# Optimization experiments

Measured on AMD Instinct MI355X. Metric: run time of the kernel, lower is better.

Reference implementation:

```python
import jax, jax.numpy as jnp
import numpy as np

L, D, H, T, B = 4, 512, 8, 1024, 8
FF = 4 * D          # 2048
E = 2
EC = E * D          # 1024 conv channels
K = 31
W = 64              # attention window
DH = D // H
EPS = 1e-5


def _ln(x, g, b):
    m = jnp.mean(x, axis=-1, keepdims=True)
    v = jnp.mean((x - m) ** 2, axis=-1, keepdims=True)
    return (x - m) * jax.lax.rsqrt(v + EPS) * g + b


def setup_inputs() -> dict:
    key = jax.random.key(0)
    ks = iter(jax.random.split(key, 64))
    n = lambda shape, s=0.02: jax.random.normal(next(ks), shape, dtype=jnp.float32) * s
    inp = {
        'x': jax.random.normal(next(ks), (B, T, D), dtype=jnp.float32),
        # FFN1 (half residual)
        'ffn1_ln_g': jnp.ones((L, D)), 'ffn1_ln_b': jnp.zeros((L, D)),
        'ffn1_w1': n((L, D, FF)), 'ffn1_b1': jnp.zeros((L, FF)),
        'ffn1_w2': n((L, FF, D)), 'ffn1_b2': jnp.zeros((L, D)),
        # local MHSA
        'attn_ln_g': jnp.ones((L, D)), 'attn_ln_b': jnp.zeros((L, D)),
        'qkv_w': n((L, D, 3 * D)), 'qkv_b': jnp.zeros((L, 3 * D)),
        'outp_w': n((L, D, D)), 'outp_b': jnp.zeros((L, D)),
        # conv module
        'conv_ln_g': jnp.ones((L, D)), 'conv_ln_b': jnp.zeros((L, D)),
        'pw1_w': n((L, D, 2 * EC)), 'pw1_b': jnp.zeros((L, 2 * EC)),
        'dw_w': n((L, EC, 1, K), 0.1), 'dw_b': jnp.zeros((L, EC)),
        'gn_g': jnp.ones((L, EC)), 'gn_b': jnp.zeros((L, EC)),
        'pw2_w': n((L, EC, D)), 'pw2_b': jnp.zeros((L, D)),
        # FFN2 (half residual)
        'ffn2_ln_g': jnp.ones((L, D)), 'ffn2_ln_b': jnp.zeros((L, D)),
        'ffn2_w1': n((L, D, FF)), 'ffn2_b1': jnp.zeros((L, FF)),
        'ffn2_w2': n((L, FF, D)), 'ffn2_b2': jnp.zeros((L, D)),
        # per-block final LN and decoder final LN
        'blk_ln_g': jnp.ones((L, D)), 'blk_ln_b': jnp.zeros((L, D)),
        'final_ln_g': jnp.ones((D,)), 'final_ln_b': jnp.zeros((D,)),
    }
    return inp


def _forward(x, ffn1_ln_g, ffn1_ln_b, ffn1_w1, ffn1_b1, ffn1_w2, ffn1_b2,
             attn_ln_g, attn_ln_b, qkv_w, qkv_b, outp_w, outp_b,
             conv_ln_g, conv_ln_b, pw1_w, pw1_b, dw_w, dw_b, gn_g, gn_b, pw2_w, pw2_b,
             ffn2_ln_g, ffn2_ln_b, ffn2_w1, ffn2_b1, ffn2_w2, ffn2_b2,
             blk_ln_g, blk_ln_b, final_ln_g, final_ln_b):
    t = jnp.arange(T)
    local_ok = jnp.abs(t[:, None] - t[None, :]) <= (W // 2)   # [T,T] banded window mask
    scale = DH ** -0.5

    for l in range(L):
        # ---- FFN1 (half residual), SiLU ----
        h = _ln(x, ffn1_ln_g[l], ffn1_ln_b[l])
        h = jax.nn.silu(h @ ffn1_w1[l] + ffn1_b1[l]) @ ffn1_w2[l] + ffn1_b2[l]
        x = x + 0.5 * h

        # ---- local windowed MHSA ----
        a = _ln(x, attn_ln_g[l], attn_ln_b[l])
        qkv = (a @ qkv_w[l] + qkv_b[l]).reshape(B, T, 3, H, DH)
        q, k, v = (qkv[:, :, 0].transpose(0, 2, 1, 3),  # [B,H,T,DH]
                   qkv[:, :, 1].transpose(0, 2, 1, 3),
                   qkv[:, :, 2].transpose(0, 2, 1, 3))
        scores = jnp.einsum('bhqd,bhkd->bhqk', q, k) * scale
        scores = jnp.where(local_ok, scores, -jnp.inf)
        attn = jax.nn.softmax(scores, axis=-1)
        o = jnp.einsum('bhqk,bhkd->bhqd', attn, v)
        o = o.transpose(0, 2, 1, 3).reshape(B, T, D)
        x = x + (o @ outp_w[l] + outp_b[l])

        # ---- convolution module ----
        c = _ln(x, conv_ln_g[l], conv_ln_b[l])
        c = c @ pw1_w[l] + pw1_b[l]                 # [B,T,2EC]
        c = c[..., :EC] * jax.nn.sigmoid(c[..., EC:])  # GLU (channel halves)
        c = c.transpose(0, 2, 1)                    # [B,EC,T]
        c = jax.lax.conv_general_dilated(
            c, dw_w[l], window_strides=(1,), padding=[((K - 1) // 2, (K - 1) // 2)],
            dimension_numbers=('NCH', 'OIH', 'NCH'), feature_group_count=EC)
        c = c + dw_b[l][None, :, None]
        # GroupNorm(num_groups=1): normalize over (C,T) per sample
        m = jnp.mean(c, axis=(1, 2), keepdims=True)
        vv = jnp.mean((c - m) ** 2, axis=(1, 2), keepdims=True)
        c = (c - m) * jax.lax.rsqrt(vv + EPS) * gn_g[l][None, :, None] + gn_b[l][None, :, None]
        c = jax.nn.silu(c)
        c = c.transpose(0, 2, 1) @ pw2_w[l] + pw2_b[l]  # [B,T,D]
        x = x + c

        # ---- FFN2 (half residual) ----
        h = _ln(x, ffn2_ln_g[l], ffn2_ln_b[l])
        h = jax.nn.silu(h @ ffn2_w1[l] + ffn2_b1[l]) @ ffn2_w2[l] + ffn2_b2[l]
        x = x + 0.5 * h

        # ---- per-block final LayerNorm ----
        x = _ln(x, blk_ln_g[l], blk_ln_b[l])

    return _ln(x, final_ln_g, final_ln_b)


def reference(x, ffn1_ln_g, ffn1_ln_b, ffn1_w1, ffn1_b1, ffn1_w2, ffn1_b2,
              attn_ln_g, attn_ln_b, qkv_w, qkv_b, outp_w, outp_b,
              conv_ln_g, conv_ln_b, pw1_w, pw1_b, dw_w, dw_b, gn_g, gn_b, pw2_w, pw2_b,
              ffn2_ln_g, ffn2_ln_b, ffn2_w1, ffn2_b1, ffn2_w2, ffn2_b2,
              blk_ln_g, blk_ln_b, final_ln_g, final_ln_b):
    return _forward(x, ffn1_ln_g, ffn1_ln_b, ffn1_w1, ffn1_b1, ffn1_w2, ffn1_b2,
                    attn_ln_g, attn_ln_b, qkv_w, qkv_b, outp_w, outp_b,
                    conv_ln_g, conv_ln_b, pw1_w, pw1_b, dw_w, dw_b, gn_g, gn_b, pw2_w, pw2_b,
                    ffn2_ln_g, ffn2_ln_b, ffn2_w1, ffn2_b1, ffn2_w2, ffn2_b2,
                    blk_ln_g, blk_ln_b, final_ln_g, final_ln_b)
```

## Files before the change

kernel.cpp:

```cpp
#include <hip/hip_runtime.h>
#include <hip/hip_bf16.h>
#include <math.h>

#define L_ 4
#define D_ 512
#define H_ 8
#define T_ 1024
#define B_ 8
#define FF_ 2048
#define EC_ 1024
#define KW_ 31
#define DH_ 64
#define ROWS (B_*T_)

typedef __attribute__((ext_vector_type(8))) short short8;
typedef __attribute__((ext_vector_type(4))) float f32x4;
typedef __attribute__((ext_vector_type(4))) unsigned short ushort4v;

static __device__ __forceinline__ unsigned short f2bf(float f) {
  __hip_bfloat16 h = __float2bfloat16(f);
  unsigned short u;
  __builtin_memcpy(&u, &h, 2);
  return u;
}
static __device__ __forceinline__ float bf2f(unsigned short h) {
  union { unsigned u; float f; } v; v.u = ((unsigned)h) << 16;
  return v.f;
}
static __device__ __forceinline__ float sigm(float x) {
  return __builtin_amdgcn_rcpf(1.0f + __expf(-x));
}

#define GLDS(gp, lp) __builtin_amdgcn_global_load_lds( \
    (const __attribute__((address_space(1))) unsigned int*)(const void*)(gp), \
    (__attribute__((address_space(3))) unsigned int*)(void*)(lp), 16, 0, 0)

#define SW8(row, slot) ((slot) ^ (((row) ^ ((row) >> 3)) & 7))

__global__ __launch_bounds__(256) void ln_bf16_kernel(const float* __restrict__ x,
    const float* __restrict__ g, const float* __restrict__ b, unsigned short* __restrict__ y)
{
  int row = blockIdx.x * 4 + (threadIdx.x >> 6);
  int l = threadIdx.x & 63;
  const float* xr = x + (size_t)row * D_ + l * 8;
  float4 v0 = *(const float4*)xr;
  float4 v1 = *(const float4*)(xr + 4);
  float vv[8] = {v0.x, v0.y, v0.z, v0.w, v1.x, v1.y, v1.z, v1.w};
  float s = 0.f, s2 = 0.f;
#pragma unroll
  for (int j = 0; j < 8; ++j) { s += vv[j]; s2 += vv[j] * vv[j]; }
#pragma unroll
  for (int off = 32; off; off >>= 1) {
    s  += __shfl_xor(s,  off, 64);
    s2 += __shfl_xor(s2, off, 64);
  }
  float mean = s * (1.0f / D_);
  float var  = s2 * (1.0f / D_) - mean * mean;
  float r = __builtin_amdgcn_rsqf(var + 1e-5f);
  float4 g0 = *(const float4*)(g + l * 8);
  float4 g1 = *(const float4*)(g + l * 8 + 4);
  float4 b0 = *(const float4*)(b + l * 8);
  float4 b1 = *(const float4*)(b + l * 8 + 4);
  float gg[8] = {g0.x, g0.y, g0.z, g0.w, g1.x, g1.y, g1.z, g1.w};
  float bb[8] = {b0.x, b0.y, b0.z, b0.w, b1.x, b1.y, b1.z, b1.w};
  short8 o;
#pragma unroll
  for (int j = 0; j < 8; ++j) o[j] = (short)f2bf((vv[j] - mean) * r * gg[j] + bb[j]);
  *(short8*)(y + (size_t)row * D_ + l * 8) = o;
}

template<bool BF2>
__global__ __launch_bounds__(256) void ln_dual_kernel(const float* __restrict__ x,
    const float* __restrict__ g1, const float* __restrict__ b1,
    const float* __restrict__ g2, const float* __restrict__ b2,
    float* __restrict__ y1, void* __restrict__ y2)
{
  int row = blockIdx.x * 4 + (threadIdx.x >> 6);
  int l = threadIdx.x & 63;
  const float* xr = x + (size_t)row * D_ + l * 8;
  float4 v0 = *(const float4*)xr;
  float4 v1 = *(const float4*)(xr + 4);
  float vv[8] = {v0.x, v0.y, v0.z, v0.w, v1.x, v1.y, v1.z, v1.w};
  float s = 0.f, s2 = 0.f;
#pragma unroll
  for (int j = 0; j < 8; ++j) { s += vv[j]; s2 += vv[j] * vv[j]; }
#pragma unroll
  for (int off = 32; off; off >>= 1) {
    s  += __shfl_xor(s,  off, 64);
    s2 += __shfl_xor(s2, off, 64);
  }
  float mean = s * (1.0f / D_);
  float var  = s2 * (1.0f / D_) - mean * mean;
  float r = __builtin_amdgcn_rsqf(var + 1e-5f);
  float4 g0 = *(const float4*)(g1 + l * 8);
  float4 g1v = *(const float4*)(g1 + l * 8 + 4);
  float4 b0 = *(const float4*)(b1 + l * 8);
  float4 b1v = *(const float4*)(b1 + l * 8 + 4);
  float ga[8] = {g0.x, g0.y, g0.z, g0.w, g1v.x, g1v.y, g1v.z, g1v.w};
  float ba[8] = {b0.x, b0.y, b0.z, b0.w, b1v.x, b1v.y, b1v.z, b1v.w};
  float yv[8];
  float u = 0.f, u2 = 0.f;
#pragma unroll
  for (int j = 0; j < 8; ++j) {
    yv[j] = (vv[j] - mean) * r * ga[j] + ba[j];
    u += yv[j]; u2 += yv[j] * yv[j];
  }
  {
    float4 o0 = {yv[0], yv[1], yv[2], yv[3]};
    float4 o1 = {yv[4], yv[5], yv[6], yv[7]};
    float* yp = y1 + (size_t)row * D_ + l * 8;
    *(float4*)yp = o0; *(float4*)(yp + 4) = o1;
  }
#pragma unroll
  for (int off = 32; off; off >>= 1) {
    u  += __shfl_xor(u,  off, 64);
    u2 += __shfl_xor(u2, off, 64);
  }
  float mean2 = u * (1.0f / D_);
  float var2  = u2 * (1.0f / D_) - mean2 * mean2;
  float r2 = __builtin_amdgcn_rsqf(var2 + 1e-5f);
  float4 c0 = *(const float4*)(g2 + l * 8);
  float4 c1 = *(const float4*)(g2 + l * 8 + 4);
  float4 d0 = *(const float4*)(b2 + l * 8);
  float4 d1 = *(const float4*)(b2 + l * 8 + 4);
  float gc[8] = {c0.x, c0.y, c0.z, c0.w, c1.x, c1.y, c1.z, c1.w};
  float bc[8] = {d0.x, d0.y, d0.z, d0.w, d1.x, d1.y, d1.z, d1.w};
  if constexpr (BF2) {
    short8 o;
#pragma unroll
    for (int j = 0; j < 8; ++j) o[j] = (short)f2bf((yv[j] - mean2) * r2 * gc[j] + bc[j]);
    *(short8*)((unsigned short*)y2 + (size_t)row * D_ + l * 8) = o;
  } else {
    float z[8];
#pragma unroll
    for (int j = 0; j < 8; ++j) z[j] = (yv[j] - mean2) * r2 * gc[j] + bc[j];
    float4 o0 = {z[0], z[1], z[2], z[3]};
    float4 o1 = {z[4], z[5], z[6], z[7]};
    float* yp = (float*)y2 + (size_t)row * D_ + l * 8;
    *(float4*)yp = o0; *(float4*)(yp + 4) = o1;
  }
}

__global__ __launch_bounds__(256) void wtr_kernel(const float* __restrict__ W,
    unsigned short* __restrict__ Wt, int K, int N)
{
  __shared__ float tile[32][33];
  const float* Wl = W + (size_t)blockIdx.z * K * N;
  unsigned short* Wtl = Wt + (size_t)blockIdx.z * K * N;
  int n0 = blockIdx.x * 32, k0 = blockIdx.y * 32;
  int c = threadIdx.x & 31, r = threadIdx.x >> 5;
#pragma unroll
  for (int it = 0; it < 4; ++it) {
    int kk = r + it * 8;
    tile[kk][c] = Wl[(size_t)(k0 + kk) * N + n0 + c];
  }
  __syncthreads();
#pragma unroll
  for (int it = 0; it < 4; ++it) {
    int nn = r + it * 8;
    Wtl[(size_t)(n0 + nn) * K + k0 + c] = f2bf(tile[c][nn]);
  }
}

template<int EPI>
__global__ __launch_bounds__(256) void gemm_mfma(
    const unsigned short* __restrict__ A, const unsigned short* __restrict__ Wt,
    const float* __restrict__ bias, void* __restrict__ Cv,
    int N, int K)
{
  constexpr int TM = 128;
  constexpr int AI = TM / 32;
  __shared__ __align__(16) unsigned short As[3][TM * 32];
  __shared__ __align__(16) unsigned short Bs[3][128 * 32];
  int t = threadIdx.x;
  int gx = gridDim.x;
  int nwg = gx * gridDim.y;
  int orig = blockIdx.y * gx + blockIdx.x;
  int lg = (orig & 7) * (nwg >> 3) + (orig >> 3);
  int row0 = (lg / gx) * TM;
  int col0 = (lg % gx) * (EPI == 3 ? 64 : 128);
  int l = t & 63, w = t >> 6, wm = w >> 1, wn = w & 1;

  int ar0 = t >> 2;
  int sa0 = (t & 3) ^ ((ar0 >> 1) & 3);
  int ar1 = (t + 256) >> 2;
  int sa1 = (t & 3) ^ ((ar1 >> 1) & 3);
  const unsigned short* agp0 = A + (size_t)(row0 + ar0) * K + sa0 * 8;
  const unsigned short* agp1 = A + (size_t)(row0 + ar1) * K + sa1 * 8;
  const unsigned short* bgp0 = Wt + (size_t)(col0 + ar0) * K + sa0 * 8;
  const unsigned short* bgp1 =
      (EPI == 3) ? Wt + (size_t)(EC_ + col0 + (ar1 - 64)) * K + sa1 * 8
                 : Wt + (size_t)(col0 + ar1) * K + sa1 * 8;

  int lrow = (l >> 4) * 4, lcol = l & 15, kq = l >> 4;
  int aoff[AI], boff[4];
#pragma unroll
  for (int i = 0; i < AI; ++i) {
    int row = wm * (TM / 2) + i * 16 + lcol;
    aoff[i] = (row * 4 + (kq ^ ((row >> 1) & 3))) * 8;
  }
#pragma unroll
  for (int j = 0; j < 4; ++j) {
    int row;
    if constexpr (EPI == 3)
      row = (j < 2 ? wn * 32 + j * 16 : 64 + wn * 32 + (j - 2) * 16) + lcol;
    else
      row = wn * 64 + j * 16 + lcol;
    boff[j] = (row * 4 + (kq ^ ((row >> 1) & 3))) * 8;
  }

  f32x4 acc[AI][4] = {};
  int nt = K >> 5;

  auto stage = [&](int buf) {
    GLDS(agp0, As[buf] + t * 8);
    GLDS(agp1, As[buf] + (t + 256) * 8);
    GLDS(bgp0, Bs[buf] + t * 8);
    GLDS(bgp1, Bs[buf] + (t + 256) * 8);
    agp0 += 32; agp1 += 32; bgp0 += 32; bgp1 += 32;
  };
  stage(0); stage(1);
  int cur = 0, nxt = 2;

  for (int kt = 0; kt < nt; ++kt) {
    if (kt < nt - 1) asm volatile("s_waitcnt vmcnt(4)" ::: "memory");
    else             asm volatile("s_waitcnt vmcnt(0)" ::: "memory");
    __builtin_amdgcn_s_barrier();
    __builtin_amdgcn_sched_barrier(0);
    if (kt + 2 < nt) { stage(nxt); nxt = (nxt == 2) ? 0 : nxt + 1; }
    const unsigned short* Ab = As[cur];
    const unsigned short* Bb = Bs[cur];
    cur = (cur == 2) ? 0 : cur + 1;
    short8 af[AI], bfr[4];
#pragma unroll
    for (int i = 0; i < AI; ++i) af[i]  = *(const short8*)(Ab + aoff[i]);
#pragma unroll
    for (int j = 0; j < 4; ++j) bfr[j] = *(const short8*)(Bb + boff[j]);
    __builtin_amdgcn_s_setprio(1);
#pragma unroll
    for (int i = 0; i < AI; ++i)
#pragma unroll
      for (int j = 0; j < 4; ++j)
        acc[i][j] = __builtin_amdgcn_mfma_f32_16x16x32_bf16(af[i], bfr[j], acc[i][j], 0, 0, 0);
    __builtin_amdgcn_s_setprio(0);
  }

  if constexpr (EPI == 3) {
    float bja[2], bjg[2];
#pragma unroll
    for (int j = 0; j < 2; ++j) {
      int c = col0 + wn * 32 + j * 16 + lcol;
      bja[j] = bias[c];
      bjg[j] = bias[EC_ + c];
    }
#pragma unroll
    for (int i = 0; i < AI; ++i) {
      int gr0 = row0 + wm * (TM / 2) + i * 16 + lrow;
#pragma unroll
      for (int j = 0; j < 2; ++j) {
        int gc = col0 + wn * 32 + j * 16 + lcol;
#pragma unroll
        for (int q = 0; q < 4; ++q) {
          float a = acc[i][j][q] + bja[j];
          float g = acc[i][j + 2][q] + bjg[j];
          ((unsigned short*)Cv)[(size_t)(gr0 + q) * N + gc] = f2bf(a * sigm(g));
        }
      }
    }
  } else {
    float bj[4];
#pragma unroll
    for (int j = 0; j < 4; ++j) bj[j] = bias[col0 + wn * 64 + j * 16 + lcol];
#pragma unroll
    for (int i = 0; i < AI; ++i) {
      int gr0 = row0 + wm * (TM / 2) + i * 16 + lrow;
#pragma unroll
      for (int j = 0; j < 4; ++j) {
        int gc = col0 + wn * 64 + j * 16 + lcol;
#pragma unroll
        for (int q = 0; q < 4; ++q) {
          float v = acc[i][j][q] + bj[j];
          size_t off = (size_t)(gr0 + q) * N + gc;
          if constexpr (EPI == 0) {
            ((unsigned short*)Cv)[off] = f2bf(v);
          } else {
            ((unsigned short*)Cv)[off] = f2bf(v * sigm(v));
          }
        }
      }
    }
  }
}

__global__ __launch_bounds__(256) void gemm_res64(
    const unsigned short* __restrict__ A, const unsigned short* __restrict__ Wt,
    const float* __restrict__ bias, const float* __restrict__ R, float* __restrict__ C,
    int N, int K, float alpha)
{
  __shared__ __align__(16) unsigned short As[3][64 * 64];
  __shared__ __align__(16) unsigned short Bs[3][128 * 64];
  int t = threadIdx.x;
  int gx = gridDim.x;
  int nwg = gx * gridDim.y;
  int orig = blockIdx.y * gx + blockIdx.x;
  int lg = (orig & 7) * (nwg >> 3) + (orig >> 3);
  int row0 = (lg / gx) * 64;
  int col0 = (lg % gx) * 128;
  int l = t & 63, w = t >> 6, wm = w >> 1, wn = w & 1;

  int arA0 = t >> 3;
  int sA0  = (t & 7) ^ (arA0 & 7);
  int cA1  = t + 256;
  int arA1 = cA1 >> 3;
  int sA1  = (cA1 & 7) ^ (arA1 & 7);
  const unsigned short* agp0 = A + (size_t)(row0 + arA0) * K + sA0 * 8;
  const unsigned short* agp1 = A + (size_t)(row0 + arA1) * K + sA1 * 8;
  const unsigned short* bgp[4];
#pragma unroll
  for (int q = 0; q < 4; ++q) {
    int c = t + q * 256;
    int r = c >> 3, s = (c & 7) ^ (r & 7);
    bgp[q] = Wt + (size_t)(col0 + r) * K + s * 8;
  }

  int lcol = l & 15, kq = l >> 4, lrow = kq * 4;
  int aoff[2][2], boff[4][2];
#pragma unroll
  for (int i = 0; i < 2; ++i) {
    int row = wm * 32 + i * 16 + lcol;
#pragma unroll
    for (int kk = 0; kk < 2; ++kk)
      aoff[i][kk] = row * 64 + (((kk * 4 + kq) ^ (row & 7)) * 8);
  }
#pragma unroll
  for (int j = 0; j < 4; ++j) {
    int row = wn * 64 + j * 16 + lcol;
#pragma unroll
    for (int kk = 0; kk < 2; ++kk)
      boff[j][kk] = row * 64 + (((kk * 4 + kq) ^ (row & 7)) * 8);
  }

  f32x4 acc[2][4] = {};
  int nt = K >> 6;

  auto stage = [&](int buf) {
    GLDS(agp0, As[buf] + t * 8);
    GLDS(agp1, As[buf] + (t + 256) * 8);
#pragma unroll
    for (int q = 0; q < 4; ++q) GLDS(bgp[q], Bs[buf] + (t + q * 256) * 8);
    agp0 += 64; agp1 += 64;
#pragma unroll
    for (int q = 0; q < 4; ++q) bgp[q] += 64;
  };
  stage(0); stage(1);
  int cur = 0, nxt = 2;

  for (int kt = 0; kt < nt; ++kt) {
    if (kt < nt - 1) asm volatile("s_waitcnt vmcnt(6)" ::: "memory");
    else             asm volatile("s_waitcnt vmcnt(0)" ::: "memory");
    __builtin_amdgcn_s_barrier();
    __builtin_amdgcn_sched_barrier(0);
    if (kt + 2 < nt) { stage(nxt); nxt = (nxt == 2) ? 0 : nxt + 1; }
    const unsigned short* Ab = As[cur];
    const unsigned short* Bb = Bs[cur];
    cur = (cur == 2) ? 0 : cur + 1;
    short8 af[2][2], bfr[4][2];
#pragma unroll
    for (int i = 0; i < 2; ++i)
#pragma unroll
      for (int kk = 0; kk < 2; ++kk) af[i][kk] = *(const short8*)(Ab + aoff[i][kk]);
#pragma unroll
    for (int j = 0; j < 4; ++j)
#pragma unroll
      for (int kk = 0; kk < 2; ++kk) bfr[j][kk] = *(const short8*)(Bb + boff[j][kk]);
    __builtin_amdgcn_s_setprio(1);
#pragma unroll
    for (int kk = 0; kk < 2; ++kk)
#pragma unroll
      for (int i = 0; i < 2; ++i)
#pragma unroll
        for (int j = 0; j < 4; ++j)
          acc[i][j] = __builtin_amdgcn_mfma_f32_16x16x32_bf16(af[i][kk], bfr[j][kk],
                                                              acc[i][j], 0, 0, 0);
    __builtin_amdgcn_s_setprio(0);
  }

  float bj[4];
#pragma unroll
  for (int j = 0; j < 4; ++j) bj[j] = bias[col0 + wn * 64 + j * 16 + lcol];
#pragma unroll
  for (int i = 0; i < 2; ++i) {
    int gr0 = row0 + wm * 32 + i * 16 + lrow;
#pragma unroll
    for (int j = 0; j < 4; ++j) {
      int gc = col0 + wn * 64 + j * 16 + lcol;
#pragma unroll
      for (int q = 0; q < 4; ++q) {
        size_t off = (size_t)(gr0 + q) * N + gc;
        C[off] = R[off] + alpha * (acc[i][j][q] + bj[j]);
      }
    }
  }
}

__global__ __launch_bounds__(256) void attn_kernel(const unsigned short* __restrict__ QKV,
                                                   unsigned short* __restrict__ O)
{
  __shared__ __align__(16) unsigned short Ks[128 * 64];
  __shared__ __align__(16) unsigned short Vt[64 * 128];
  __shared__ __align__(16) unsigned short Ps[64 * 128];
  int qt = blockIdx.x, h = blockIdx.y, b = blockIdx.z;
  int t = threadIdx.x;
  int l = t & 63, w = t >> 6;
  int q0 = qt * 64;
  int jbase = q0 - 32;

#pragma unroll
  for (int i = 0; i < 4; ++i) {
    int c = t + i * 256;
    int row = c >> 3, sl = c & 7;
    int jg = jbase + row;
    short8 kv = {};
    if ((unsigned)jg < (unsigned)T_)
      kv = *(const short8*)(QKV + ((size_t)(b * T_ + jg)) * 1536 + 512 + h * DH_ + sl * 8);
    *(short8*)(Ks + row * 64 + SW8(row, sl) * 8) = kv;
  }
#pragma unroll
  for (int i = 0; i < 4; ++i) {
    int c = t + i * 256;
    int row = c >> 3, d0 = (c & 7) * 8;
    int jg = jbase + row;
    short8 vv = {};
    if ((unsigned)jg < (unsigned)T_)
      vv = *(const short8*)(QKV + ((size_t)(b * T_ + jg)) * 1536 + 1024 + h * DH_ + d0);
#pragma unroll
    for (int q = 0; q < 8; ++q) {
      int d = d0 + q;
      Vt[d * 128 + SW8(d, row >> 3) * 8 + (row & 7)] = (unsigned short)vv[q];
    }
  }
  short8 qf[2];
#pragma unroll
  for (int ks = 0; ks < 2; ++ks)
    qf[ks] = *(const short8*)(QKV + ((size_t)(b * T_ + q0 + w * 16 + (l & 15))) * 1536
                              + h * DH_ + ks * 32 + (l >> 4) * 8);
  __syncthreads();

  f32x4 sacc[8] = {};
#pragma unroll
  for (int jt = 0; jt < 8; ++jt) {
#pragma unroll
    for (int ks = 0; ks < 2; ++ks) {
      int row = jt * 16 + (l & 15);
      int sl = ks * 4 + (l >> 4);
      short8 kf = *(const short8*)(Ks + row * 64 + SW8(row, sl) * 8);
      sacc[jt] = __builtin_amdgcn_mfma_f32_16x16x32_bf16(qf[ks], kf, sacc[jt], 0, 0, 0);
    }
  }

  const float scale = 0.125f;
  int qgl0 = q0 + w * 16 + ((l >> 4) << 2);
  int jl = jbase + (l & 15);
  float m4[4] = {-3.0e38f, -3.0e38f, -3.0e38f, -3.0e38f};
#pragma unroll
  for (int jt = 0; jt < 8; ++jt) {
#pragma unroll
    for (int r = 0; r < 4; ++r) {
      float s = sacc[jt][r] * scale;
      int jg = jl + jt * 16;
      int dd = jg - (qgl0 + r);
      bool ok = ((unsigned)jg < (unsigned)T_) && (dd <= 32) && (dd >= -32);
      s = ok ? s : -3.0e38f;
      sacc[jt][r] = s;
      m4[r] = fmaxf(m4[r], s);
    }
  }
#pragma unroll
  for (int r = 0; r < 4; ++r) {
    m4[r] = fmaxf(m4[r], __shfl_xor(m4[r], 1, 64));
    m4[r] = fmaxf(m4[r], __shfl_xor(m4[r], 2, 64));
    m4[r] = fmaxf(m4[r], __shfl_xor(m4[r], 4, 64));
    m4[r] = fmaxf(m4[r], __shfl_xor(m4[r], 8, 64));
  }
  float sum4[4] = {0.f, 0.f, 0.f, 0.f};
#pragma unroll
  for (int jt = 0; jt < 8; ++jt) {
#pragma unroll
    for (int r = 0; r < 4; ++r) {
      float e = __expf(sacc[jt][r] - m4[r]);
      sum4[r] += e;
      int qrow = w * 16 + ((l >> 4) << 2) + r;
      int j = jt * 16 + (l & 15);
      Ps[qrow * 128 + SW8(qrow, j >> 3) * 8 + (j & 7)] = f2bf(e);
    }
  }
#pragma unroll
  for (int r = 0; r < 4; ++r) {
    sum4[r] += __shfl_xor(sum4[r], 1, 64);
    sum4[r] += __shfl_xor(sum4[r], 2, 64);
    sum4[r] += __shfl_xor(sum4[r], 4, 64);
    sum4[r] += __shfl_xor(sum4[r], 8, 64);
    sum4[r] = __builtin_amdgcn_rcpf(sum4[r]);
  }

  f32x4 oacc[4] = {};
#pragma unroll
  for (int ks = 0; ks < 4; ++ks) {
    int prow = w * 16 + (l & 15);
    int sl = ks * 4 + (l >> 4);
    short8 pf = *(const short8*)(Ps + prow * 128 + SW8(prow, sl) * 8);
#pragma unroll
    for (int dt = 0; dt < 4; ++dt) {
      int vrow = dt * 16 + (l & 15);
      short8 vf = *(const short8*)(Vt + vrow * 128 + SW8(vrow, sl) * 8);
      oacc[dt] = __builtin_amdgcn_mfma_f32_16x16x32_bf16(pf, vf, oacc[dt], 0, 0, 0);
    }
  }
#pragma unroll
  for (int dt = 0; dt < 4; ++dt) {
#pragma unroll
    for (int r = 0; r < 4; ++r) {
      int qg = q0 + w * 16 + ((l >> 4) << 2) + r;
      int d = dt * 16 + (l & 15);
      O[((size_t)(b * T_ + qg)) * D_ + h * DH_ + d] = f2bf(oacc[dt][r] * sum4[r]);
    }
  }
}

#define TT_ 16
__global__ __launch_bounds__(256) void dwconv_kernel(const unsigned short* __restrict__ X,
    const float* __restrict__ w, const float* __restrict__ bias, float* __restrict__ Y,
    float* __restrict__ red)
{
  int t = threadIdx.x;
  int gid = blockIdx.x;
  int ecb = gid & 3;
  int tt  = (gid >> 2) & 63;
  int b   = gid >> 8;
  int e  = ecb * 256 + t;
  int t0 = tt * TT_;
  const unsigned short* xp = X + (size_t)b * T_ * EC_ + e;

  float wr[KW_];
#pragma unroll
  for (int k = 0; k < KW_; ++k) wr[k] = w[e * KW_ + k];
  float out[TT_];
  float bv = bias[e];
#pragma unroll
  for (int i = 0; i < TT_; ++i) out[i] = bv;

#pragma unroll
  for (int j = 0; j < TT_ + KW_ - 1; ++j) {
    int tj = t0 - 15 + j;
    float xv = ((unsigned)tj < (unsigned)T_) ? bf2f(xp[(size_t)tj * EC_]) : 0.f;
#pragma unroll
    for (int i = 0; i < TT_; ++i) {
      int k = j - i;
      if (k >= 0 && k < KW_) out[i] = fmaf(xv, wr[k], out[i]);
    }
  }
  float* yp = Y + ((size_t)b * T_ + t0) * EC_ + e;
  float s = 0.f, s2 = 0.f;
#pragma unroll
  for (int i = 0; i < TT_; ++i) {
    yp[(size_t)i * EC_] = out[i];
    s += out[i]; s2 += out[i] * out[i];
  }
#pragma unroll
  for (int off = 32; off; off >>= 1) {
    s  += __shfl_down(s,  off, 64);
    s2 += __shfl_down(s2, off, 64);
  }
  __shared__ float rs[4], rq[4];
  if ((t & 63) == 0) { rs[t >> 6] = s; rq[t >> 6] = s2; }
  __syncthreads();
  if (t == 0) {
    int loc = gid & 255;
    red[(b * 256 + loc) * 2]     = rs[0] + rs[1] + rs[2] + rs[3];
    red[(b * 256 + loc) * 2 + 1] = rq[0] + rq[1] + rq[2] + rq[3];
  }
}

__global__ __launch_bounds__(256) void gn_stats_kernel(const float* __restrict__ partial,
                                                       float* __restrict__ stats)
{
  int b = blockIdx.x, t = threadIdx.x;
  float s  = partial[b * 512 + t * 2];
  float s2 = partial[b * 512 + t * 2 + 1];
#pragma unroll
  for (int off = 32; off; off >>= 1) {
    s  += __shfl_down(s,  off, 64);
    s2 += __shfl_down(s2, off, 64);
  }
  __shared__ float rs[4], rq[4];
  if ((t & 63) == 0) { rs[t >> 6] = s; rq[t >> 6] = s2; }
  __syncthreads();
  if (t == 0) {
    float S = rs[0] + rs[1] + rs[2] + rs[3];
    float S2 = rq[0] + rq[1] + rq[2] + rq[3];
    const float n = (float)(T_ * EC_);
    float mean = S / n;
    float var  = S2 / n - mean * mean;
    stats[b * 2]     = mean;
    stats[b * 2 + 1] = __builtin_amdgcn_rsqf(var + 1e-5f);
  }
}

__global__ __launch_bounds__(256) void gn_apply_kernel(const float* __restrict__ X,
    const float* __restrict__ stats, const float* __restrict__ g, const float* __restrict__ bb,
    unsigned short* __restrict__ out)
{
  int idx = blockIdx.x * 256 + threadIdx.x;
  int e4 = (idx & 255) << 2;
  int bt = idx >> 8;
  int b  = bt >> 10;
  float mean = stats[b * 2], rstd = stats[b * 2 + 1];
  float4 v  = *(const float4*)(X + (size_t)idx * 4);
  float4 gv = *(const float4*)(g + e4);
  float4 bv = *(const float4*)(bb + e4);
  float vv[4] = {v.x, v.y, v.z, v.w};
  float gg[4] = {gv.x, gv.y, gv.z, gv.w};
  float bbv[4] = {bv.x, bv.y, bv.z, bv.w};
  ushort4v o;
#pragma unroll
  for (int j = 0; j < 4; ++j) {
    float u = (vv[j] - mean) * rstd * gg[j] + bbv[j];
    o[j] = f2bf(u * sigm(u));
  }
  *(ushort4v*)(out + (size_t)idx * 4) = o;
}

extern "C" void kernel_launch(void* const* d_in, const int* in_sizes, int n_in,
                              void* d_out, int out_size, void* d_ws, size_t ws_size,
                              hipStream_t stream)
{
  const float* in_x      = (const float*)d_in[0];
  const float* ffn1_ln_g = (const float*)d_in[1];
  const float* ffn1_ln_b = (const float*)d_in[2];
  const float* ffn1_w1   = (const float*)d_in[3];
  const float* ffn1_b1   = (const float*)d_in[4];
  const float* ffn1_w2   = (const float*)d_in[5];
  const float* ffn1_b2   = (const float*)d_in[6];
  const float* attn_ln_g = (const float*)d_in[7];
  const float* attn_ln_b = (const float*)d_in[8];
  const float* qkv_w     = (const float*)d_in[9];
  const float* qkv_b     = (const float*)d_in[10];
  const float* outp_w    = (const float*)d_in[11];
  const float* outp_b    = (const float*)d_in[12];
  const float* conv_ln_g = (const float*)d_in[13];
  const float* conv_ln_b = (const float*)d_in[14];
  const float* pw1_w     = (const float*)d_in[15];
  const float* pw1_b     = (const float*)d_in[16];
  const float* dw_w      = (const float*)d_in[17];
  const float* dw_b      = (const float*)d_in[18];
  const float* gn_g      = (const float*)d_in[19];
  const float* gn_b      = (const float*)d_in[20];
  const float* pw2_w     = (const float*)d_in[21];
  const float* pw2_b     = (const float*)d_in[22];
  const float* ffn2_ln_g = (const float*)d_in[23];
  const float* ffn2_ln_b = (const float*)d_in[24];
  const float* ffn2_w1   = (const float*)d_in[25];
  const float* ffn2_b1   = (const float*)d_in[26];
  const float* ffn2_w2   = (const float*)d_in[27];
  const float* ffn2_b2   = (const float*)d_in[28];
  const float* blk_ln_g  = (const float*)d_in[29];
  const float* blk_ln_b  = (const float*)d_in[30];
  const float* fin_ln_g  = (const float*)d_in[31];
  const float* fin_ln_b  = (const float*)d_in[32];

  char* p = (char*)d_ws;
  float* x    = (float*)p;          p += (size_t)ROWS * D_ * 4;
  float* big3 = (float*)p;          p += (size_t)ROWS * EC_ * 4;
  float* red  = (float*)p;          p += 8192 * 4;
  unsigned short* abuf  = (unsigned short*)p; p += (size_t)ROWS * D_ * 2;
  unsigned short* inner = (unsigned short*)p; p += (size_t)ROWS * FF_ * 2;
  unsigned short* big2  = (unsigned short*)p; p += (size_t)ROWS * EC_ * 2;
  unsigned short* wt_w1a = (unsigned short*)p; p += (size_t)L_ * D_ * FF_ * 2;
  unsigned short* wt_w1b = (unsigned short*)p; p += (size_t)L_ * FF_ * D_ * 2;
  unsigned short* wt_qkv = (unsigned short*)p; p += (size_t)L_ * D_ * 1536 * 2;
  unsigned short* wt_out = (unsigned short*)p; p += (size_t)L_ * D_ * D_ * 2;
  unsigned short* wt_pw1 = (unsigned short*)p; p += (size_t)L_ * D_ * 2048 * 2;
  unsigned short* wt_pw2 = (unsigned short*)p; p += (size_t)L_ * EC_ * D_ * 2;
  unsigned short* wt_w2a = (unsigned short*)p; p += (size_t)L_ * D_ * FF_ * 2;
  unsigned short* wt_w2b = (unsigned short*)p; p += (size_t)L_ * FF_ * D_ * 2;
  float* stats = red + 4096;

  hipMemcpyAsync(x, in_x, sizeof(float) * (size_t)ROWS * D_,
                 hipMemcpyDeviceToDevice, stream);

  dim3 blk256(256);
  wtr_kernel<<<dim3(FF_/32,  D_/32,  L_), blk256, 0, stream>>>(ffn1_w1, wt_w1a, D_, FF_);
  wtr_kernel<<<dim3(D_/32,   FF_/32, L_), blk256, 0, stream>>>(ffn1_w2, wt_w1b, FF_, D_);
  wtr_kernel<<<dim3(1536/32, D_/32,  L_), blk256, 0, stream>>>(qkv_w,   wt_qkv, D_, 1536);
  wtr_kernel<<<dim3(D_/32,   D_/32,  L_), blk256, 0, stream>>>(outp_w,  wt_out, D_, D_);
  wtr_kernel<<<dim3(2048/32, D_/32,  L_), blk256, 0, stream>>>(pw1_w,   wt_pw1, D_, 2048);
  wtr_kernel<<<dim3(D_/32,   EC_/32, L_), blk256, 0, stream>>>(pw2_w,   wt_pw2, EC_, D_);
  wtr_kernel<<<dim3(FF_/32,  D_/32,  L_), blk256, 0, stream>>>(ffn2_w1, wt_w2a, D_, FF_);
  wtr_kernel<<<dim3(D_/32,   FF_/32, L_), blk256, 0, stream>>>(ffn2_w2, wt_w2b, FF_, D_);

  ln_bf16_kernel<<<ROWS/4, blk256, 0, stream>>>(x, ffn1_ln_g, ffn1_ln_b, abuf);

  for (int l = 0; l < L_; ++l) {
    gemm_mfma<1><<<dim3(FF_/128, ROWS/128), blk256, 0, stream>>>(
        abuf, wt_w1a + (size_t)l*D_*FF_, ffn1_b1 + l*FF_, inner, FF_, D_);
    gemm_res64<<<dim3(D_/128, ROWS/64), blk256, 0, stream>>>(
        inner, wt_w1b + (size_t)l*FF_*D_, ffn1_b2 + l*D_, x, x, D_, FF_, 0.5f);

    ln_bf16_kernel<<<ROWS/4, blk256, 0, stream>>>(x, attn_ln_g + l*D_, attn_ln_b + l*D_, abuf);
    gemm_mfma<0><<<dim3(1536/128, ROWS/128), blk256, 0, stream>>>(
        abuf, wt_qkv + (size_t)l*D_*1536, qkv_b + l*1536, inner, 1536, D_);
    attn_kernel<<<dim3(T_/64, H_, B_), blk256, 0, stream>>>(inner, abuf);
    gemm_res64<<<dim3(D_/128, ROWS/64), blk256, 0, stream>>>(
        abuf, wt_out + (size_t)l*D_*D_, outp_b + l*D_, x, x, D_, D_, 1.0f);

    ln_bf16_kernel<<<ROWS/4, blk256, 0, stream>>>(x, conv_ln_g + l*D_, conv_ln_b + l*D_, abuf);
    gemm_mfma<3><<<dim3(EC_/64, ROWS/128), blk256, 0, stream>>>(
        abuf, wt_pw1 + (size_t)l*D_*2048, pw1_b + l*2048, big2, EC_, D_);
    dwconv_kernel<<<B_ * (T_/TT_) * (EC_/256), blk256, 0, stream>>>(
        big2, dw_w + (size_t)l*EC_*KW_, dw_b + l*EC_, big3, red);
    gn_stats_kernel<<<B_, blk256, 0, stream>>>(red, stats);
    gn_apply_kernel<<<(ROWS * EC_ / 4) / 256, blk256, 0, stream>>>(
        big3, stats, gn_g + l*EC_, gn_b + l*EC_, big2);
    gemm_res64<<<dim3(D_/128, ROWS/64), blk256, 0, stream>>>(
        big2, wt_pw2 + (size_t)l*EC_*D_, pw2_b + l*D_, x, x, D_, EC_, 1.0f);

    ln_bf16_kernel<<<ROWS/4, blk256, 0, stream>>>(x, ffn2_ln_g + l*D_, ffn2_ln_b + l*D_, abuf);
    gemm_mfma<1><<<dim3(FF_/128, ROWS/128), blk256, 0, stream>>>(
        abuf, wt_w2a + (size_t)l*D_*FF_, ffn2_b1 + l*FF_, inner, FF_, D_);
    gemm_res64<<<dim3(D_/128, ROWS/64), blk256, 0, stream>>>(
        inner, wt_w2b + (size_t)l*FF_*D_, ffn2_b2 + l*D_, x, x, D_, FF_, 0.5f);

    if (l < L_ - 1) {
      ln_dual_kernel<true><<<ROWS/4, blk256, 0, stream>>>(
          x, blk_ln_g + l*D_, blk_ln_b + l*D_,
          ffn1_ln_g + (l+1)*D_, ffn1_ln_b + (l+1)*D_, x, abuf);
    } else {
      ln_dual_kernel<false><<<ROWS/4, blk256, 0, stream>>>(
          x, blk_ln_g + l*D_, blk_ln_b + l*D_, fin_ln_g, fin_ln_b, x, d_out);
    }
  }
}
```

Measured before the change: 1.197 ms.

## Store residual stream and depthwise-conv output in bf16 instead of fp32

The residual activation x, the dual-LN outputs and the depthwise-conv output buffer are now kept in bf16 rather than fp32. The LN kernels, the residual GEMM epilogue, dwconv and groupnorm-apply read and write bf16. This halves memory traffic on these bandwidth-bound passes, and the initial device copy is replaced by a conversion kernel. The cost is that the residual stream accumulates in bf16, so rounding error grows across layers and the result may drift from the fp32 reference.

New measurement: 1.150 ms. -3.9%, faster.

```diff
diff --git a/kernel.cpp b/kernel.cpp
--- a/kernel.cpp
+++ b/kernel.cpp
@@ -37,15 +37,28 @@
 
 #define SW8(row, slot) ((slot) ^ (((row) ^ ((row) >> 3)) & 7))
 
-__global__ __launch_bounds__(256) void ln_bf16_kernel(const float* __restrict__ x,
+__global__ __launch_bounds__(256) void cvt_kernel(const float* __restrict__ in,
+                                                  unsigned short* __restrict__ out)
+{
+  size_t i = ((size_t)blockIdx.x * 256 + threadIdx.x) * 8;
+  float4 v0 = *(const float4*)(in + i);
+  float4 v1 = *(const float4*)(in + i + 4);
+  float vv[8] = {v0.x, v0.y, v0.z, v0.w, v1.x, v1.y, v1.z, v1.w};
+  short8 o;
+#pragma unroll
+  for (int j = 0; j < 8; ++j) o[j] = (short)f2bf(vv[j]);
+  *(short8*)(out + i) = o;
+}
+
+__global__ __launch_bounds__(256) void ln_bf16_kernel(const unsigned short* __restrict__ x,
     const float* __restrict__ g, const float* __restrict__ b, unsigned short* __restrict__ y)
 {
   int row = blockIdx.x * 4 + (threadIdx.x >> 6);
   int l = threadIdx.x & 63;
-  const float* xr = x + (size_t)row * D_ + l * 8;
-  float4 v0 = *(const float4*)xr;
-  float4 v1 = *(const float4*)(xr + 4);
-  float vv[8] = {v0.x, v0.y, v0.z, v0.w, v1.x, v1.y, v1.z, v1.w};
+  short8 xr = *(const short8*)(x + (size_t)row * D_ + l * 8);
+  float vv[8];
+#pragma unroll
+  for (int j = 0; j < 8; ++j) vv[j] = bf2f((unsigned short)xr[j]);
   float s = 0.f, s2 = 0.f;
 #pragma unroll
   for (int j = 0; j < 8; ++j) { s += vv[j]; s2 += vv[j] * vv[j]; }
@@ -70,17 +83,17 @@
 }
 
 template<bool BF2>
-__global__ __launch_bounds__(256) void ln_dual_kernel(const float* __restrict__ x,
+__global__ __launch_bounds__(256) void ln_dual_kernel(const unsigned short* __restrict__ x,
     const float* __restrict__ g1, const float* __restrict__ b1,
     const float* __restrict__ g2, const float* __restrict__ b2,
-    float* __restrict__ y1, void* __restrict__ y2)
+    unsigned short* __restrict__ y1, void* __restrict__ y2)
 {
   int row = blockIdx.x * 4 + (threadIdx.x >> 6);
   int l = threadIdx.x & 63;
-  const float* xr = x + (size_t)row * D_ + l * 8;
-  float4 v0 = *(const float4*)xr;
-  float4 v1 = *(const float4*)(xr + 4);
-  float vv[8] = {v0.x, v0.y, v0.z, v0.w, v1.x, v1.y, v1.z, v1.w};
+  short8 xr = *(const short8*)(x + (size_t)row * D_ + l * 8);
+  float vv[8];
+#pragma unroll
+  for (int j = 0; j < 8; ++j) vv[j] = bf2f((unsigned short)xr[j]);
   float s = 0.f, s2 = 0.f;
 #pragma unroll
   for (int j = 0; j < 8; ++j) { s += vv[j]; s2 += vv[j] * vv[j]; }
@@ -106,10 +119,10 @@
     u += yv[j]; u2 += yv[j] * yv[j];
   }
   {
-    float4 o0 = {yv[0], yv[1], yv[2], yv[3]};
-    float4 o1 = {yv[4], yv[5], yv[6], yv[7]};
-    float* yp = y1 + (size_t)row * D_ + l * 8;
-    *(float4*)yp = o0; *(float4*)(yp + 4) = o1;
+    short8 o;
+#pragma unroll
+    for (int j = 0; j < 8; ++j) o[j] = (short)f2bf(yv[j]);
+    *(short8*)(y1 + (size_t)row * D_ + l * 8) = o;
   }
 #pragma unroll
   for (int off = 32; off; off >>= 1) {
@@ -294,8 +307,8 @@
 
 __global__ __launch_bounds__(256) void gemm_res64(
     const unsigned short* __restrict__ A, const unsigned short* __restrict__ Wt,
-    const float* __restrict__ bias, const float* __restrict__ R, float* __restrict__ C,
-    int N, int K, float alpha)
+    const float* __restrict__ bias, const unsigned short* __restrict__ R,
+    unsigned short* __restrict__ C, int N, int K, float alpha)
 {
   __shared__ __align__(16) unsigned short As[3][64 * 64];
   __shared__ __align__(16) unsigned short Bs[3][128 * 64];
@@ -397,7 +410,7 @@
 #pragma unroll
       for (int q = 0; q < 4; ++q) {
         size_t off = (size_t)(gr0 + q) * N + gc;
-        C[off] = R[off] + alpha * (acc[i][j][q] + bj[j]);
+        C[off] = f2bf(bf2f(R[off]) + alpha * (acc[i][j][q] + bj[j]));
       }
     }
   }
@@ -529,8 +542,8 @@
 
 #define TT_ 16
 __global__ __launch_bounds__(256) void dwconv_kernel(const unsigned short* __restrict__ X,
-    const float* __restrict__ w, const float* __restrict__ bias, float* __restrict__ Y,
-    float* __restrict__ red)
+    const float* __restrict__ w, const float* __restrict__ bias,
+    unsigned short* __restrict__ Y, float* __restrict__ red)
 {
   int t = threadIdx.x;
   int gid = blockIdx.x;
@@ -559,11 +572,11 @@
       if (k >= 0 && k < KW_) out[i] = fmaf(xv, wr[k], out[i]);
     }
   }
-  float* yp = Y + ((size_t)b * T_ + t0) * EC_ + e;
+  unsigned short* yp = Y + ((size_t)b * T_ + t0) * EC_ + e;
   float s = 0.f, s2 = 0.f;
 #pragma unroll
   for (int i = 0; i < TT_; ++i) {
-    yp[(size_t)i * EC_] = out[i];
+    yp[(size_t)i * EC_] = f2bf(out[i]);
     s += out[i]; s2 += out[i] * out[i];
   }
 #pragma unroll
@@ -606,7 +619,7 @@
   }
 }
 
-__global__ __launch_bounds__(256) void gn_apply_kernel(const float* __restrict__ X,
+__global__ __launch_bounds__(256) void gn_apply_kernel(const unsigned short* __restrict__ X,
     const float* __restrict__ stats, const float* __restrict__ g, const float* __restrict__ bb,
     unsigned short* __restrict__ out)
 {
@@ -615,16 +628,15 @@
   int bt = idx >> 8;
   int b  = bt >> 10;
   float mean = stats[b * 2], rstd = stats[b * 2 + 1];
-  float4 v  = *(const float4*)(X + (size_t)idx * 4);
+  ushort4v v = *(const ushort4v*)(X + (size_t)idx * 4);
   float4 gv = *(const float4*)(g + e4);
   float4 bv = *(const float4*)(bb + e4);
-  float vv[4] = {v.x, v.y, v.z, v.w};
   float gg[4] = {gv.x, gv.y, gv.z, gv.w};
   float bbv[4] = {bv.x, bv.y, bv.z, bv.w};
   ushort4v o;
 #pragma unroll
   for (int j = 0; j < 4; ++j) {
-    float u = (vv[j] - mean) * rstd * gg[j] + bbv[j];
+    float u = (bf2f(v[j]) - mean) * rstd * gg[j] + bbv[j];
     o[j] = f2bf(u * sigm(u));
   }
   *(ushort4v*)(out + (size_t)idx * 4) = o;
@@ -669,8 +681,8 @@
   const float* fin_ln_b  = (const float*)d_in[32];
 
   char* p = (char*)d_ws;
-  float* x    = (float*)p;          p += (size_t)ROWS * D_ * 4;
-  float* big3 = (float*)p;          p += (size_t)ROWS * EC_ * 4;
+  unsigned short* x    = (unsigned short*)p; p += (size_t)ROWS * D_ * 2;
+  unsigned short* big3 = (unsigned short*)p; p += (size_t)ROWS * EC_ * 2;
   float* red  = (float*)p;          p += 8192 * 4;
   unsigned short* abuf  = (unsigned short*)p; p += (size_t)ROWS * D_ * 2;
   unsigned short* inner = (unsigned short*)p; p += (size_t)ROWS * FF_ * 2;
@@ -685,10 +697,9 @@
   unsigned short* wt_w2b = (unsigned short*)p; p += (size_t)L_ * FF_ * D_ * 2;
   float* stats = red + 4096;
 
-  hipMemcpyAsync(x, in_x, sizeof(float) * (size_t)ROWS * D_,
-                 hipMemcpyDeviceToDevice, stream);
-
   dim3 blk256(256);
+  cvt_kernel<<<ROWS * D_ / (256 * 8), blk256, 0, stream>>>(in_x, x);
+
   wtr_kernel<<<dim3(FF_/32,  D_/32,  L_), blk256, 0, stream>>>(ffn1_w1, wt_w1a, D_, FF_);
   wtr_kernel<<<dim3(D_/32,   FF_/32, L_), blk256, 0, stream>>>(ffn1_w2, wt_w1b, FF_, D_);
   wtr_kernel<<<dim3(1536/32, D_/32,  L_), blk256, 0, stream>>>(qkv_w,   wt_qkv, D_, 1536);
```
